# Optimization experiments

Hardware: AMD Instinct MI355X
Metric: run time of the kernel (lower is better)

## Reference

```python
import jax, jax.numpy as jnp
import numpy as np

B, S, P, L, H = 64, 512, 32, 30, 768
FH = 1024  # fc_hidden_size


def setup_inputs() -> dict:
    key = jax.random.key(0)
    ks = jax.random.split(key, 8)
    token_embeddings = jax.random.normal(ks[0], (B, S, H), jnp.float32)
    pooler_output = jax.random.normal(ks[1], (B, H), jnp.float32)
    num_positions = jax.random.randint(ks[2], (B, P), 0, S)
    # labels: 0/1 codes, with trailing slots per example padded with -1 rows
    lab = jax.random.randint(ks[3], (B, P, L), 0, 2).astype(jnp.float32)
    valid = jax.random.randint(ks[4], (B, 1), 8, P + 1)  # num real slots per example
    row = jnp.arange(P)[None, :]
    lab = jnp.where((row < valid)[:, :, None], lab, -1.0)
    num_codes_labels = lab.reshape(B, P * L)
    W1 = jax.random.normal(ks[5], (2 * H, FH), jnp.float32) / np.sqrt(2 * H)
    b1 = jnp.zeros((FH,), jnp.float32)
    W2 = jax.random.normal(ks[6], (FH, FH // 2), jnp.float32) / np.sqrt(FH)
    b2 = jnp.zeros((FH // 2,), jnp.float32)
    W3 = jax.random.normal(ks[7], (FH // 2, L), jnp.float32) / np.sqrt(FH // 2)
    b3 = jnp.zeros((L,), jnp.float32)
    return {"token_embeddings": token_embeddings, "pooler_output": pooler_output,
            "num_positions": num_positions, "num_codes_labels": num_codes_labels,
            "W1": W1, "b1": b1, "W2": W2, "b2": b2, "W3": W3, "b3": b3}


def reference(token_embeddings, pooler_output, num_positions, num_codes_labels,
              W1, b1, W2, b2, W3, b3):
    # gather number-token hidden states: [B, P, H]
    p_hidden = jnp.take_along_axis(token_embeddings, num_positions[:, :, None], axis=1)
    feat = jnp.concatenate(
        [p_hidden, jnp.broadcast_to(pooler_output[:, None, :], p_hidden.shape)], axis=-1)
    # Batch_Net_CLS head. NOTE: original uses nn.LeakyReLU(True) -> negative_slope=1.0,
    # which is mathematically the identity, so the activations are omitted (faithful).
    h = feat @ W1 + b1
    h = h @ W2 + b2
    logits = h @ W3 + b3  # [B, P, L]

    labels = num_codes_labels.reshape(B, -1, L)
    pad_pre = jnp.any(labels != -1.0, axis=-1)  # [B, P] True for real slots
    mf = pad_pre.astype(jnp.float32)

    # BCEWithLogitsLoss over non-pad elements: softplus(x) - x*y, mean
    bce_elem = jax.nn.softplus(logits) - logits * labels
    bce_loss = jnp.sum(bce_elem * mf[:, :, None]) / (jnp.sum(mf) * L)

    binary = (jax.nn.sigmoid(logits) > 0.5).astype(jnp.float32)
    count_out = jnp.sum(binary, axis=-1)
    count_lab = jnp.sum(labels, axis=-1)
    count_loss = jnp.mean((count_out - count_lab) ** 2 * mf)

    # position loss: only slots where both counts are exactly 1 (single-hot)
    eq = (count_out == 1.0) & (count_lab == 1.0)
    pos_out = jnp.argmax(binary, axis=-1).astype(jnp.float32)
    pos_lab = jnp.argmax(labels, axis=-1).astype(jnp.float32)
    n_eq = jnp.sum(eq.astype(jnp.float32))
    pos_sum = jnp.sum((pos_out - pos_lab) ** 2 * eq.astype(jnp.float32))
    position_loss = jnp.where(n_eq > 0, pos_sum / jnp.maximum(n_eq, 1.0), 0.0)

    return bce_loss + 10.0 * count_loss + 5.0 * position_loss
```

## Files before the change

kernel.cpp:

```cpp
#include <hip/hip_runtime.h>
#include <cstddef>
#include <cstdint>

#define Mq   2048
#define Lq   30
#define N1q  1024
#define N2q  512
#define K1q  1536
#define Hq   768
#define NBLK 512

typedef float    f32x4 __attribute__((ext_vector_type(4)));
typedef _Float16 f16x8 __attribute__((ext_vector_type(8)));

#define GLD16(gptr, lptr) \
  __builtin_amdgcn_global_load_lds((const __attribute__((address_space(1))) void*)(gptr), \
                                   (__attribute__((address_space(3))) void*)(lptr), 16, 0, 0)

__device__ void transpose_tile(const float* __restrict__ src,
                               _Float16* __restrict__ dst,
                               int K, int N, int k0, int n0) {
  __shared__ float T[64][65];
  const int t = threadIdx.x;
  {
    const int kl = t >> 2, nc = (t & 3) * 16;
    const float* s = src + (size_t)(k0 + kl) * N + n0 + nc;
    float4 v0 = *(const float4*)s;
    float4 v1 = *(const float4*)(s + 4);
    float4 v2 = *(const float4*)(s + 8);
    float4 v3 = *(const float4*)(s + 12);
    T[nc + 0][kl] = v0.x; T[nc + 1][kl] = v0.y; T[nc + 2][kl] = v0.z; T[nc + 3][kl] = v0.w;
    T[nc + 4][kl] = v1.x; T[nc + 5][kl] = v1.y; T[nc + 6][kl] = v1.z; T[nc + 7][kl] = v1.w;
    T[nc + 8][kl] = v2.x; T[nc + 9][kl] = v2.y; T[nc +10][kl] = v2.z; T[nc +11][kl] = v2.w;
    T[nc +12][kl] = v3.x; T[nc +13][kl] = v3.y; T[nc +14][kl] = v3.z; T[nc +15][kl] = v3.w;
  }
  __syncthreads();
  {
    const int nl = t >> 2, kc = (t & 3) * 16;
    __align__(16) _Float16 tmp[16];
    #pragma unroll
    for (int i = 0; i < 16; ++i) tmp[i] = (_Float16)T[nl][kc + i];
    _Float16* d = dst + (size_t)(n0 + nl) * K + k0 + kc;
    *(uint4*)d       = *(const uint4*)tmp;
    *(uint4*)(d + 8) = *(const uint4*)(tmp + 8);
  }
}

__global__ __launch_bounds__(256)
void prep_all(const float* __restrict__ tok, const float* __restrict__ pool,
              const int* __restrict__ npos, const float* __restrict__ W1,
              const float* __restrict__ W2, _Float16* __restrict__ A1,
              _Float16* __restrict__ W1T, _Float16* __restrict__ W2T) {
  const int bid = blockIdx.x, tid = threadIdx.x;
  if (bid < 256) {
    const int q = tid >> 5, l32 = tid & 31;
    const int m = bid * 8 + q;
    const int bI = m >> 5, p = m & 31;
    const int pos = npos[bI * 32 + p];
    const float* src1 = tok + ((size_t)bI * 512 + pos) * Hq;
    const float* src2 = pool + (size_t)bI * Hq;
    _Float16* dst = A1 + (size_t)m * K1q;
    for (int g = l32; g < 384; g += 32) {
      const float* s = (g < 192) ? (src1 + g * 4) : (src2 + (g - 192) * 4);
      float4 v = *(const float4*)s;
      __align__(8) _Float16 o[4] = {(_Float16)v.x, (_Float16)v.y, (_Float16)v.z, (_Float16)v.w};
      *(uint2*)(dst + g * 4) = *(const uint2*)o;
    }
  } else if (bid < 640) {
    const int idx = bid - 256;
    transpose_tile(W1, W1T, K1q, N1q, (idx / 16) * 64, (idx % 16) * 64);
  } else {
    const int idx = bid - 640;
    transpose_tile(W2, W2T, N1q, N2q, (idx / 8) * 64, (idx % 8) * 64);
  }
}

__global__ __launch_bounds__(256)
void gemm1_k(const _Float16* __restrict__ A, const _Float16* __restrict__ BT,
             const float* __restrict__ b1, _Float16* __restrict__ C1) {
  __shared__ _Float16 As[2][64 * 64];
  __shared__ _Float16 Bs[2][64 * 64];
  const int tid = threadIdx.x, w = tid >> 6, lane = tid & 63;
  const int n0 = blockIdx.x * 64, m0 = blockIdx.y * 64;
  const int ml = lane & 15, g4 = lane >> 4;
  const int wm = (w >> 1) * 32, wn = (w & 1) * 32;
  const int lr = lane >> 3, lc = lane & 7;

  f32x4 acc[2][2];
  #pragma unroll
  for (int i = 0; i < 2; ++i)
    #pragma unroll
    for (int j = 0; j < 2; ++j)
      #pragma unroll
      for (int r = 0; r < 4; ++r) acc[i][j][r] = 0.f;

  auto stage = [&](int it, int b) {
    const int kt = it * 64;
    #pragma unroll
    for (int t = 0; t < 2; ++t) {
      const int r  = w * 16 + t * 8 + lr;
      const int cs = lc ^ (r & 7);
      GLD16(A  + (size_t)(m0 + r) * K1q + kt + cs * 8, &As[b][(w * 16 + t * 8) * 64]);
      GLD16(BT + (size_t)(n0 + r) * K1q + kt + cs * 8, &Bs[b][(w * 16 + t * 8) * 64]);
    }
  };

  stage(0, 0);
  __syncthreads();
  #pragma unroll 1
  for (int it = 0; it < 24; ++it) {
    const int cur = it & 1;
    if (it < 23) stage(it + 1, cur ^ 1);
    f16x8 af[2][2], bf[2][2];
    #pragma unroll
    for (int i = 0; i < 2; ++i) {
      const int ar = wm + i * 16 + ml;
      const int br = wn + i * 16 + ml;
      #pragma unroll
      for (int ks = 0; ks < 2; ++ks) {
        af[i][ks] = *(const f16x8*)&As[cur][ar * 64 + (((ks * 4 + g4) ^ (ar & 7)) << 3)];
        bf[i][ks] = *(const f16x8*)&Bs[cur][br * 64 + (((ks * 4 + g4) ^ (br & 7)) << 3)];
      }
    }
    #pragma unroll
    for (int i = 0; i < 2; ++i)
      #pragma unroll
      for (int j = 0; j < 2; ++j)
        #pragma unroll
        for (int ks = 0; ks < 2; ++ks)
          acc[i][j] = __builtin_amdgcn_mfma_f32_16x16x32_f16(bf[j][ks], af[i][ks], acc[i][j], 0, 0, 0);
    __syncthreads();
  }

  #pragma unroll
  for (int i = 0; i < 2; ++i) {
    const int row = m0 + wm + i * 16 + ml;
    #pragma unroll
    for (int j = 0; j < 2; ++j) {
      const int col = n0 + wn + j * 16 + g4 * 4;
      const float4 bv = *(const float4*)(b1 + col);
      __align__(8) _Float16 o[4] = {(_Float16)(acc[i][j][0] + bv.x),
                                    (_Float16)(acc[i][j][1] + bv.y),
                                    (_Float16)(acc[i][j][2] + bv.z),
                                    (_Float16)(acc[i][j][3] + bv.w)};
      *(uint2*)(C1 + (size_t)row * N1q + col) = *(const uint2*)o;
    }
  }
}

__global__ __launch_bounds__(256)
void gemm2_k(const _Float16* __restrict__ A, const _Float16* __restrict__ BT,
             const float* __restrict__ b2, float* __restrict__ C2) {
  __shared__ _Float16 As[2][32 * 64];
  __shared__ _Float16 Bs[2][64 * 64];
  const int tid = threadIdx.x, w = tid >> 6, lane = tid & 63;
  const int n0 = blockIdx.x * 64, m0 = blockIdx.y * 32;
  const int ml = lane & 15, g4 = lane >> 4;
  const int wm = (w & 1) * 16, wn = (w >> 1) * 32;
  const int lr = lane >> 3, lc = lane & 7;

  f32x4 acc[2];
  #pragma unroll
  for (int j = 0; j < 2; ++j)
    #pragma unroll
    for (int r = 0; r < 4; ++r) acc[j][r] = 0.f;

  auto stage = [&](int it, int b) {
    const int kt = it * 64;
    {
      const int r  = w * 8 + lr;
      const int cs = lc ^ (r & 7);
      GLD16(A + (size_t)(m0 + r) * N1q + kt + cs * 8, &As[b][(w * 8) * 64]);
    }
    #pragma unroll
    for (int t = 0; t < 2; ++t) {
      const int r  = w * 16 + t * 8 + lr;
      const int cs = lc ^ (r & 7);
      GLD16(BT + (size_t)(n0 + r) * N1q + kt + cs * 8, &Bs[b][(w * 16 + t * 8) * 64]);
    }
  };

  stage(0, 0);
  __syncthreads();
  #pragma unroll 1
  for (int it = 0; it < 16; ++it) {
    const int cur = it & 1;
    if (it < 15) stage(it + 1, cur ^ 1);
    f16x8 af[2], bf[2][2];
    {
      const int ar = wm + ml;
      #pragma unroll
      for (int ks = 0; ks < 2; ++ks)
        af[ks] = *(const f16x8*)&As[cur][ar * 64 + (((ks * 4 + g4) ^ (ar & 7)) << 3)];
    }
    #pragma unroll
    for (int j = 0; j < 2; ++j) {
      const int br = wn + j * 16 + ml;
      #pragma unroll
      for (int ks = 0; ks < 2; ++ks)
        bf[j][ks] = *(const f16x8*)&Bs[cur][br * 64 + (((ks * 4 + g4) ^ (br & 7)) << 3)];
    }
    #pragma unroll
    for (int j = 0; j < 2; ++j)
      #pragma unroll
      for (int ks = 0; ks < 2; ++ks)
        acc[j] = __builtin_amdgcn_mfma_f32_16x16x32_f16(bf[j][ks], af[ks], acc[j], 0, 0, 0);
    __syncthreads();
  }

  const int row = m0 + wm + ml;
  #pragma unroll
  for (int j = 0; j < 2; ++j) {
    const int col = n0 + wn + j * 16 + g4 * 4;
    const float4 bv = *(const float4*)(b2 + col);
    float4 o;
    o.x = acc[j][0] + bv.x; o.y = acc[j][1] + bv.y;
    o.z = acc[j][2] + bv.z; o.w = acc[j][3] + bv.w;
    *(float4*)(C2 + (size_t)row * N2q + col) = o;
  }
}

__global__ __launch_bounds__(256)
void loss_kernel(const float* __restrict__ C2, const float* __restrict__ W3,
                 const float* __restrict__ b3, const float* __restrict__ labels,
                 float* __restrict__ part) {
  __shared__ float hrow[4][512];
  __shared__ float red[4][5];
  const int tid = threadIdx.x, w = tid >> 6, lane = tid & 63;
  const int m = blockIdx.x * 4 + w;

  {
    const int k = lane * 8;
    const float* cp = C2 + (size_t)m * N2q + k;
    *(float4*)&hrow[w][k]     = *(const float4*)cp;
    *(float4*)&hrow[w][k + 4] = *(const float4*)(cp + 4);
  }
  __syncthreads();

  const int c  = lane & 31;
  const int kh = lane >> 5;
  float a0 = 0.f, a1 = 0.f, a2 = 0.f, a3 = 0.f;
  if (c < Lq) {
    const float* hp = hrow[w] + kh * 256;
    const float* wp = W3 + (size_t)(kh * 256) * Lq + c;
    #pragma unroll 4
    for (int i = 0; i < 256; i += 4) {
      a0 = fmaf(hp[i],     wp[(i)     * Lq], a0);
      a1 = fmaf(hp[i + 1], wp[(i + 1) * Lq], a1);
      a2 = fmaf(hp[i + 2], wp[(i + 2) * Lq], a2);
      a3 = fmaf(hp[i + 3], wp[(i + 3) * Lq], a3);
    }
  }
  float a = (a0 + a1) + (a2 + a3);
  a += __shfl_xor(a, 32);

  const bool act = lane < Lq;
  float logit = 0.f, lab = 0.f;
  if (act) {
    logit = a + b3[lane];
    lab = labels[(size_t)m * Lq + lane];
  }

  const unsigned long long validmask = __ballot(act && lab != -1.0f);
  const unsigned long long outmask   = __ballot(act && logit > 0.0f);
  const unsigned long long labmask   = __ballot(act && lab == 1.0f);
  const bool valid = (validmask != 0ULL);
  const int count_out = __popcll(outmask);
  const int count_lab = __popcll(labmask);

  float bce = 0.f;
  if (act && valid) {
    const float x = logit;
    bce = fmaxf(x, 0.f) + log1pf(expf(-fabsf(x))) - x * lab;
  }
  bce += __shfl_xor(bce, 16); bce += __shfl_xor(bce, 8);
  bce += __shfl_xor(bce, 4);  bce += __shfl_xor(bce, 2);
  bce += __shfl_xor(bce, 1);

  if (lane == 0) {
    float pb = 0.f, pv = 0.f, pc = 0.f, pe = 0.f, pp = 0.f;
    if (valid) {
      pb = bce; pv = 1.f;
      const float d = (float)count_out - (float)count_lab;
      pc = d * d;
    }
    if (count_out == 1 && count_lab == 1) {
      const float po = (float)(__ffsll((long long)outmask) - 1);
      const float pl = (float)(__ffsll((long long)labmask) - 1);
      pe = 1.f;
      const float dp = po - pl;
      pp = dp * dp;
    }
    red[w][0] = pb; red[w][1] = pv; red[w][2] = pc; red[w][3] = pe; red[w][4] = pp;
  }
  __syncthreads();
  if (tid < 5) {
    part[blockIdx.x * 5 + tid] =
        red[0][tid] + red[1][tid] + red[2][tid] + red[3][tid];
  }
}

__global__ __launch_bounds__(256)
void finalize_kernel(const float* __restrict__ part, float* __restrict__ out) {
  __shared__ float red[32][5];
  const int t = threadIdx.x;
  if (t < 160) {
    const int j = t % 5, grp = t / 5;
    float s = 0.f;
    for (int i = grp; i < NBLK; i += 32) s += part[i * 5 + j];
    red[grp][j] = s;
  }
  __syncthreads();
  if (t == 0) {
    float t0 = 0.f, t1 = 0.f, t2 = 0.f, t3 = 0.f, t4 = 0.f;
    #pragma unroll
    for (int g = 0; g < 32; ++g) {
      t0 += red[g][0]; t1 += red[g][1]; t2 += red[g][2];
      t3 += red[g][3]; t4 += red[g][4];
    }
    const float bce = t0 / (t1 * (float)Lq);
    const float cnt = 10.0f * t2 / (float)Mq;
    const float pos = (t3 > 0.f) ? 5.0f * t4 / fmaxf(t3, 1.0f) : 0.f;
    out[0] = bce + cnt + pos;
  }
}

extern "C" void kernel_launch(void* const* d_in, const int* in_sizes, int n_in,
                              void* d_out, int out_size, void* d_ws, size_t ws_size,
                              hipStream_t stream) {
  const float* tok    = (const float*)d_in[0];
  const float* pool   = (const float*)d_in[1];
  const int*   npos   = (const int*)  d_in[2];
  const float* labels = (const float*)d_in[3];
  const float* W1     = (const float*)d_in[4];
  const float* b1     = (const float*)d_in[5];
  const float* W2     = (const float*)d_in[6];
  const float* b2     = (const float*)d_in[7];
  const float* W3     = (const float*)d_in[8];
  const float* b3     = (const float*)d_in[9];
  float* out = (float*)d_out;

  char* ws = (char*)d_ws;
  _Float16* A1   = (_Float16*)(ws + 0x00000000);
  _Float16* W1T  = (_Float16*)(ws + 0x00600000);
  _Float16* W2T  = (_Float16*)(ws + 0x00900000);
  _Float16* C1   = (_Float16*)(ws + 0x00A00000);
  float*    C2   = (float*)   (ws + 0x00E00000);
  float*    part = (float*)   (ws + 0x01200000);

  prep_all<<<768, 256, 0, stream>>>(tok, pool, npos, W1, W2, A1, W1T, W2T);
  gemm1_k<<<dim3(16, 32), 256, 0, stream>>>(A1, W1T, b1, C1);
  gemm2_k<<<dim3(8, 64), 256, 0, stream>>>(C1, W2T, b2, C2);
  loss_kernel<<<NBLK, 256, 0, stream>>>(C2, W3, b3, labels, part);
  finalize_kernel<<<1, 256, 0, stream>>>(part, out);
}
```

Measured before the change: 194.2 us.

## Triple-buffer GEMM pipelines, transpose W3, fuse finalize into loss kernel

Both GEMM kernels move from double to triple LDS buffering, with explicit vmcnt waits and one barrier per iteration, so global loads run two stages ahead of compute. W3 is transposed in the prep kernel so the loss kernel reads its weights as contiguous float4 values. The separate finalize kernel is removed: the last loss block, found through an atomic counter, performs the final reduction. This cuts per-iteration syncs and a kernel launch, in exchange for more LDS use and a hand-written wait count that must match the number of loads per stage.

After: 221.9 us. +14.3%, slower.

```diff
diff --git a/kernel.cpp b/kernel.cpp
--- a/kernel.cpp
+++ b/kernel.cpp
@@ -49,8 +49,10 @@
 __global__ __launch_bounds__(256)
 void prep_all(const float* __restrict__ tok, const float* __restrict__ pool,
               const int* __restrict__ npos, const float* __restrict__ W1,
-              const float* __restrict__ W2, _Float16* __restrict__ A1,
-              _Float16* __restrict__ W1T, _Float16* __restrict__ W2T) {
+              const float* __restrict__ W2, const float* __restrict__ W3,
+              _Float16* __restrict__ A1, _Float16* __restrict__ W1T,
+              _Float16* __restrict__ W2T, float* __restrict__ W3T,
+              unsigned* __restrict__ cnt) {
   const int bid = blockIdx.x, tid = threadIdx.x;
   if (bid < 256) {
     const int q = tid >> 5, l32 = tid & 31;
@@ -69,17 +71,23 @@
   } else if (bid < 640) {
     const int idx = bid - 256;
     transpose_tile(W1, W1T, K1q, N1q, (idx / 16) * 64, (idx % 16) * 64);
-  } else {
+  } else if (bid < 768) {
     const int idx = bid - 640;
     transpose_tile(W2, W2T, N1q, N2q, (idx / 8) * 64, (idx % 8) * 64);
+  } else {
+    if (tid == 0) cnt[0] = 0u;
+    for (int idx = tid; idx < N2q * Lq; idx += 256) {
+      const int k = idx / Lq, c = idx - k * Lq;
+      W3T[(size_t)c * N2q + k] = W3[idx];
+    }
   }
 }
 
 __global__ __launch_bounds__(256)
 void gemm1_k(const _Float16* __restrict__ A, const _Float16* __restrict__ BT,
              const float* __restrict__ b1, _Float16* __restrict__ C1) {
-  __shared__ _Float16 As[2][64 * 64];
-  __shared__ _Float16 Bs[2][64 * 64];
+  __shared__ _Float16 As[3][64 * 64];
+  __shared__ _Float16 Bs[3][64 * 64];
   const int tid = threadIdx.x, w = tid >> 6, lane = tid & 63;
   const int n0 = blockIdx.x * 64, m0 = blockIdx.y * 64;
   const int ml = lane & 15, g4 = lane >> 4;
@@ -104,13 +112,7 @@
       GLD16(BT + (size_t)(n0 + r) * K1q + kt + cs * 8, &Bs[b][(w * 16 + t * 8) * 64]);
     }
   };
-
-  stage(0, 0);
-  __syncthreads();
-  #pragma unroll 1
-  for (int it = 0; it < 24; ++it) {
-    const int cur = it & 1;
-    if (it < 23) stage(it + 1, cur ^ 1);
+  auto compute = [&](int cur) {
     f16x8 af[2][2], bf[2][2];
     #pragma unroll
     for (int i = 0; i < 2; ++i) {
@@ -129,8 +131,21 @@
         #pragma unroll
         for (int ks = 0; ks < 2; ++ks)
           acc[i][j] = __builtin_amdgcn_mfma_f32_16x16x32_f16(bf[j][ks], af[i][ks], acc[i][j], 0, 0, 0);
-    __syncthreads();
-  }
+  };
+
+  stage(0, 0); stage(1, 1);
+  #pragma unroll 1
+  for (int it = 0; it < 23; ++it) {
+    asm volatile("s_waitcnt vmcnt(4)" ::: "memory");
+    __builtin_amdgcn_s_barrier();
+    __builtin_amdgcn_sched_barrier(0);
+    if (it + 2 < 24) stage(it + 2, (it + 2) % 3);
+    compute(it % 3);
+  }
+  asm volatile("s_waitcnt vmcnt(0)" ::: "memory");
+  __builtin_amdgcn_s_barrier();
+  __builtin_amdgcn_sched_barrier(0);
+  compute(23 % 3);
 
   #pragma unroll
   for (int i = 0; i < 2; ++i) {
@@ -151,8 +166,8 @@
 __global__ __launch_bounds__(256)
 void gemm2_k(const _Float16* __restrict__ A, const _Float16* __restrict__ BT,
              const float* __restrict__ b2, float* __restrict__ C2) {
-  __shared__ _Float16 As[2][32 * 64];
-  __shared__ _Float16 Bs[2][64 * 64];
+  __shared__ _Float16 As[3][32 * 64];
+  __shared__ _Float16 Bs[3][64 * 64];
   const int tid = threadIdx.x, w = tid >> 6, lane = tid & 63;
   const int n0 = blockIdx.x * 64, m0 = blockIdx.y * 32;
   const int ml = lane & 15, g4 = lane >> 4;
@@ -179,13 +194,7 @@
       GLD16(BT + (size_t)(n0 + r) * N1q + kt + cs * 8, &Bs[b][(w * 16 + t * 8) * 64]);
     }
   };
-
-  stage(0, 0);
-  __syncthreads();
-  #pragma unroll 1
-  for (int it = 0; it < 16; ++it) {
-    const int cur = it & 1;
-    if (it < 15) stage(it + 1, cur ^ 1);
+  auto compute = [&](int cur) {
     f16x8 af[2], bf[2][2];
     {
       const int ar = wm + ml;
@@ -205,8 +214,21 @@
       #pragma unroll
       for (int ks = 0; ks < 2; ++ks)
         acc[j] = __builtin_amdgcn_mfma_f32_16x16x32_f16(bf[j][ks], af[ks], acc[j], 0, 0, 0);
-    __syncthreads();
-  }
+  };
+
+  stage(0, 0); stage(1, 1);
+  #pragma unroll 1
+  for (int it = 0; it < 15; ++it) {
+    asm volatile("s_waitcnt vmcnt(3)" ::: "memory");
+    __builtin_amdgcn_s_barrier();
+    __builtin_amdgcn_sched_barrier(0);
+    if (it + 2 < 16) stage(it + 2, (it + 2) % 3);
+    compute(it % 3);
+  }
+  asm volatile("s_waitcnt vmcnt(0)" ::: "memory");
+  __builtin_amdgcn_s_barrier();
+  __builtin_amdgcn_sched_barrier(0);
+  compute(15 % 3);
 
   const int row = m0 + wm + ml;
   #pragma unroll
@@ -221,11 +243,14 @@
 }
 
 __global__ __launch_bounds__(256)
-void loss_kernel(const float* __restrict__ C2, const float* __restrict__ W3,
+void loss_kernel(const float* __restrict__ C2, const float* __restrict__ W3T,
                  const float* __restrict__ b3, const float* __restrict__ labels,
-                 float* __restrict__ part) {
+                 float* __restrict__ part, unsigned* __restrict__ cnt,
+                 float* __restrict__ out) {
   __shared__ float hrow[4][512];
   __shared__ float red[4][5];
+  __shared__ float fred[32][5];
+  __shared__ unsigned done;
   const int tid = threadIdx.x, w = tid >> 6, lane = tid & 63;
   const int m = blockIdx.x * 4 + w;
 
@@ -242,13 +267,14 @@
   float a0 = 0.f, a1 = 0.f, a2 = 0.f, a3 = 0.f;
   if (c < Lq) {
     const float* hp = hrow[w] + kh * 256;
-    const float* wp = W3 + (size_t)(kh * 256) * Lq + c;
+    const float* wp = W3T + (size_t)c * N2q + kh * 256;
     #pragma unroll 4
     for (int i = 0; i < 256; i += 4) {
-      a0 = fmaf(hp[i],     wp[(i)     * Lq], a0);
-      a1 = fmaf(hp[i + 1], wp[(i + 1) * Lq], a1);
-      a2 = fmaf(hp[i + 2], wp[(i + 2) * Lq], a2);
-      a3 = fmaf(hp[i + 3], wp[(i + 3) * Lq], a3);
+      const float4 wv = *(const float4*)(wp + i);
+      a0 = fmaf(hp[i],     wv.x, a0);
+      a1 = fmaf(hp[i + 1], wv.y, a1);
+      a2 = fmaf(hp[i + 2], wv.z, a2);
+      a3 = fmaf(hp[i + 3], wv.w, a3);
     }
   }
   float a = (a0 + a1) + (a2 + a3);
@@ -298,30 +324,34 @@
     part[blockIdx.x * 5 + tid] =
         red[0][tid] + red[1][tid] + red[2][tid] + red[3][tid];
   }
-}
-
-__global__ __launch_bounds__(256)
-void finalize_kernel(const float* __restrict__ part, float* __restrict__ out) {
-  __shared__ float red[32][5];
-  const int t = threadIdx.x;
-  if (t < 160) {
-    const int j = t % 5, grp = t / 5;
-    float s = 0.f;
-    for (int i = grp; i < NBLK; i += 32) s += part[i * 5 + j];
-    red[grp][j] = s;
-  }
-  __syncthreads();
-  if (t == 0) {
-    float t0 = 0.f, t1 = 0.f, t2 = 0.f, t3 = 0.f, t4 = 0.f;
-    #pragma unroll
-    for (int g = 0; g < 32; ++g) {
-      t0 += red[g][0]; t1 += red[g][1]; t2 += red[g][2];
-      t3 += red[g][3]; t4 += red[g][4];
-    }
-    const float bce = t0 / (t1 * (float)Lq);
-    const float cnt = 10.0f * t2 / (float)Mq;
-    const float pos = (t3 > 0.f) ? 5.0f * t4 / fmaxf(t3, 1.0f) : 0.f;
-    out[0] = bce + cnt + pos;
+  __syncthreads();
+  if (tid == 0) {
+    __threadfence();
+    const unsigned old = atomicAdd(cnt, 1u);
+    done = (old == NBLK - 1) ? 1u : 0u;
+  }
+  __syncthreads();
+  if (done) {
+    __threadfence();
+    if (tid < 160) {
+      const int j = tid % 5, grp = tid / 5;
+      float s = 0.f;
+      for (int i = grp; i < NBLK; i += 32) s += part[i * 5 + j];
+      fred[grp][j] = s;
+    }
+    __syncthreads();
+    if (tid == 0) {
+      float t0 = 0.f, t1 = 0.f, t2 = 0.f, t3 = 0.f, t4 = 0.f;
+      #pragma unroll
+      for (int g = 0; g < 32; ++g) {
+        t0 += fred[g][0]; t1 += fred[g][1]; t2 += fred[g][2];
+        t3 += fred[g][3]; t4 += fred[g][4];
+      }
+      const float bce_ = t0 / (t1 * (float)Lq);
+      const float cnt_ = 10.0f * t2 / (float)Mq;
+      const float pos_ = (t3 > 0.f) ? 5.0f * t4 / fmaxf(t3, 1.0f) : 0.f;
+      out[0] = bce_ + cnt_ + pos_;
+    }
   }
 }
 
@@ -347,10 +377,11 @@
   _Float16* C1   = (_Float16*)(ws + 0x00A00000);
   float*    C2   = (float*)   (ws + 0x00E00000);
   float*    part = (float*)   (ws + 0x01200000);
-
-  prep_all<<<768, 256, 0, stream>>>(tok, pool, npos, W1, W2, A1, W1T, W2T);
+  float*    W3T  = (float*)   (ws + 0x01210000);
+  unsigned* cnt  = (unsigned*)(ws + 0x01220000);
+
+  prep_all<<<769, 256, 0, stream>>>(tok, pool, npos, W1, W2, W3, A1, W1T, W2T, W3T, cnt);
   gemm1_k<<<dim3(16, 32), 256, 0, stream>>>(A1, W1T, b1, C1);
   gemm2_k<<<dim3(8, 64), 256, 0, stream>>>(C1, W2T, b2, C2);
-  loss_kernel<<<NBLK, 256, 0, stream>>>(C2, W3, b3, labels, part);
-  finalize_kernel<<<1, 256, 0, stream>>>(part, out);
-}
+  loss_kernel<<<NBLK, 256, 0, stream>>>(C2, W3T, b3, labels, part, cnt, out);
+}
```
